# Optimization experiments

Measured on AMD Instinct MI355X. Metric: run time of the kernel, lower is better.

## Reference

```python
import jax, jax.numpy as jnp
import numpy as np

B, S, Lb, C, CP, H = 64, 4, 64, 32, 16, 4
LN_EPS = 1e-5


def layer_norm(x, g, b):
    mu = jnp.mean(x, axis=-1, keepdims=True)
    var = jnp.mean(jnp.square(x - mu), axis=-1, keepdims=True)
    return (x - mu) * jax.lax.rsqrt(var + LN_EPS) * g + b


def mha(x, w_in, b_in, w_out, b_out, h):
    # torch nn.MultiheadAttention, batch_first, self-attention
    Bx, L, Cx = x.shape
    d = Cx // h
    qkv = x @ w_in.T + b_in                      # (Bx, L, 3C)
    q, k, v = jnp.split(qkv, 3, axis=-1)
    sp = lambda t: t.reshape(Bx, L, h, d).transpose(0, 2, 1, 3)  # (Bx,h,L,d)
    q, k, v = sp(q), sp(k), sp(v)
    scale = 1.0 / jnp.sqrt(jnp.asarray(d, x.dtype))
    attn = jax.nn.softmax(jnp.einsum('bhid,bhjd->bhij', q, k) * scale, axis=-1)
    o = jnp.einsum('bhij,bhjd->bhid', attn, v).transpose(0, 2, 1, 3).reshape(Bx, L, Cx)
    return o @ w_out.T + b_out


def setup_inputs() -> dict:
    key = jax.random.key(0)
    ks = jax.random.split(key, 20)
    g = lambda i, shape, s=0.05: (jax.random.normal(ks[i], shape, dtype=jnp.float32) * s)
    inp = {
        'chip_ctcf': jax.random.normal(ks[0], (B, Lb), dtype=jnp.float32),
        'chip_hac':  jax.random.normal(ks[1], (B, Lb), dtype=jnp.float32),
        'chip_me1':  jax.random.normal(ks[2], (B, Lb), dtype=jnp.float32),
        'chip_me3':  jax.random.normal(ks[3], (B, Lb), dtype=jnp.float32),
        'embed_w': g(4, (C, 1)), 'embed_b': g(5, (C,)),
        'pos_embed': g(6, (1, 1, Lb, C), 0.02),
        'row_in_w': g(7, (3 * C, C)), 'row_in_b': g(8, (3 * C,)),
        'row_out_w': g(9, (C, C)), 'row_out_b': g(10, (C,)),
        'row_ln_g': jnp.ones((C,), jnp.float32), 'row_ln_b': jnp.zeros((C,), jnp.float32),
        'col_in_w': g(11, (3 * C, C)), 'col_in_b': g(12, (3 * C,)),
        'col_out_w': g(13, (C, C)), 'col_out_b': g(14, (C,)),
        'col_ln_g': jnp.ones((C,), jnp.float32), 'col_ln_b': jnp.zeros((C,), jnp.float32),
        'proj_w': g(15, (CP, C * C)), 'proj_b': g(16, (CP,)),
        'pln_g': jnp.ones((CP,), jnp.float32), 'pln_b': jnp.zeros((CP,), jnp.float32),
    }
    return inp


def reference(chip_ctcf, chip_hac, chip_me1, chip_me3,
              embed_w, embed_b, pos_embed,
              row_in_w, row_in_b, row_out_w, row_out_b, row_ln_g, row_ln_b,
              col_in_w, col_in_b, col_out_w, col_out_b, col_ln_g, col_ln_b,
              proj_w, proj_b, pln_g, pln_b):
    Bv = chip_ctcf.shape[0]
    signals = jnp.stack([chip_ctcf, chip_hac, chip_me1, chip_me3], axis=1)  # (B,4,64)
    # Linear(1, C): scalar embed
    msa = signals[..., None] * embed_w[:, 0] + embed_b                      # (B,4,64,C)
    msa = msa + pos_embed
    # row attention over the 64 bins, per track
    x = msa.reshape(Bv * S, Lb, C)
    x = layer_norm(x + mha(x, row_in_w, row_in_b, row_out_w, row_out_b, H), row_ln_g, row_ln_b)
    msa = x.reshape(Bv, S, Lb, C)
    # column attention over the 4 tracks, per bin
    x = msa.transpose(0, 2, 1, 3).reshape(Bv * Lb, S, C)
    x = layer_norm(x + mha(x, col_in_w, col_in_b, col_out_w, col_out_b, H), col_ln_g, col_ln_b)
    msa = x.reshape(Bv, Lb, S, C).transpose(0, 2, 1, 3)                     # (B,4,64,C)
    # outer product of the track-mean (as written in the torch source)
    m = jnp.mean(msa, axis=1)                                               # (B,64,C)
    pair = jnp.einsum('bic,bjd->bijcd', m, m).reshape(Bv, Lb, Lb, C * C)    # (B,64,64,1024)
    nrm = jnp.sqrt(jnp.sum(jnp.square(pair), axis=-1, keepdims=True))
    pair = pair / jnp.maximum(nrm, 1e-6)                                    # F.normalize eps=1e-6
    feat = pair @ proj_w.T + proj_b                                         # (B,64,64,CP)
    feat = layer_norm(feat, pln_g, pln_b)
    feat = feat * jax.nn.sigmoid(feat)                                      # SiLU
    return feat.transpose(0, 3, 1, 2)                                       # (B,CP,64,64)
```

## Files before the change

### kernel.cpp

```cpp
#include <hip/hip_runtime.h>
#include <hip/hip_bf16.h>

#define LN_EPS 1e-5f

__device__ __forceinline__ float dot8(float4 a0, float4 a1, float4 b0, float4 b1) {
    return a0.x * b0.x + a0.y * b0.y + a0.z * b0.z + a0.w * b0.w +
           a1.x * b1.x + a1.y * b1.y + a1.z * b1.z + a1.w * b1.w;
}

__global__ __launch_bounds__(256) void k_row(
    const float* __restrict__ ctcf, const float* __restrict__ hac,
    const float* __restrict__ me1,  const float* __restrict__ me3,
    const float* __restrict__ ew,   const float* __restrict__ eb,
    const float* __restrict__ pe,
    const float* __restrict__ w_in, const float* __restrict__ b_in,
    const float* __restrict__ w_out,const float* __restrict__ b_out,
    const float* __restrict__ ln_g, const float* __restrict__ ln_b,
    float* __restrict__ msaR)
{
    __shared__ float sx[64][33];
    __shared__ float sqkv[64 * 100];
    __shared__ float so[64][33];
    __shared__ float swin[96 * 32];
    __shared__ float swout[32 * 32];
    __shared__ float sbin[96];
    __shared__ float sbout[32], sg[32], sb[32];
    __shared__ float smean[64], srstd[64];

    const int blk = blockIdx.x;
    const int s   = blk & 3;
    const int b   = blk >> 2;
    const int tid = threadIdx.x;

    const float* chip = (s == 0) ? ctcf : (s == 1) ? hac : (s == 2) ? me1 : me3;

    for (int n = tid; n < 96 * 32; n += 256) swin[n] = w_in[n];
    for (int n = tid; n < 32 * 32; n += 256) swout[n] = w_out[n];
    if (tid < 96) sbin[tid] = b_in[tid];
    if (tid < 32) {
        sbout[tid] = b_out[tid];
        sg[tid] = ln_g[tid];
        sb[tid] = ln_b[tid];
    }
    for (int n = tid; n < 2048; n += 256) {
        int l = n >> 5, c = n & 31;
        sx[l][c] = chip[b * 64 + l] * ew[c] + eb[c] + pe[l * 32 + c];
    }
    __syncthreads();

    const int l  = tid & 63;
    const int cg = tid >> 6;

    float xr[32];
#pragma unroll
    for (int c = 0; c < 32; ++c) xr[c] = sx[l][c];

#pragma unroll
    for (int i = 0; i < 24; ++i) {
        int cc = i * 4 + cg;
        const float4* wr4 = (const float4*)&swin[cc * 32];
        float acc = sbin[cc];
#pragma unroll
        for (int c4 = 0; c4 < 8; ++c4) {
            float4 wv = wr4[c4];
            acc += xr[c4 * 4 + 0] * wv.x + xr[c4 * 4 + 1] * wv.y +
                   xr[c4 * 4 + 2] * wv.z + xr[c4 * 4 + 3] * wv.w;
        }
        sqkv[l * 100 + cc] = acc;
    }
    __syncthreads();

    {
        const int h = cg;
        const float4* qp = (const float4*)&sqkv[l * 100 + h * 8];
        float4 q0 = qp[0], q1 = qp[1];
        const float scale = 0.35355339059327373f;
        float mrun = -1e30f, denom = 0.f, a[8];
#pragma unroll
        for (int dd = 0; dd < 8; ++dd) a[dd] = 0.f;
        for (int j = 0; j < 64; ++j) {
            const float4* kp = (const float4*)&sqkv[j * 100 + 32 + h * 8];
            float4 k0 = kp[0], k1 = kp[1];
            float sc = dot8(q0, q1, k0, k1) * scale;
            const float4* vp = (const float4*)&sqkv[j * 100 + 64 + h * 8];
            float4 v0 = vp[0], v1 = vp[1];
            float mnew = fmaxf(mrun, sc);
            float corr = __expf(mrun - mnew);
            float w = __expf(sc - mnew);
            denom = denom * corr + w;
            a[0] = a[0] * corr + w * v0.x;  a[1] = a[1] * corr + w * v0.y;
            a[2] = a[2] * corr + w * v0.z;  a[3] = a[3] * corr + w * v0.w;
            a[4] = a[4] * corr + w * v1.x;  a[5] = a[5] * corr + w * v1.y;
            a[6] = a[6] * corr + w * v1.z;  a[7] = a[7] * corr + w * v1.w;
            mrun = mnew;
        }
        float inv = 1.f / denom;
#pragma unroll
        for (int dd = 0; dd < 8; ++dd) so[l][h * 8 + dd] = a[dd] * inv;
    }
    __syncthreads();

    {
        float orow[32];
#pragma unroll
        for (int k = 0; k < 32; ++k) orow[k] = so[l][k];
#pragma unroll
        for (int i = 0; i < 8; ++i) {
            int c = i * 4 + cg;
            const float4* wr4 = (const float4*)&swout[c * 32];
            float acc = sbout[c] + xr[c];
#pragma unroll
            for (int k4 = 0; k4 < 8; ++k4) {
                float4 wv = wr4[k4];
                acc += orow[k4 * 4 + 0] * wv.x + orow[k4 * 4 + 1] * wv.y +
                       orow[k4 * 4 + 2] * wv.z + orow[k4 * 4 + 3] * wv.w;
            }
            sqkv[l * 100 + c] = acc;
        }
    }
    __syncthreads();

    if (tid < 64) {
        float mu = 0.f;
#pragma unroll
        for (int c = 0; c < 32; ++c) mu += sqkv[tid * 100 + c];
        mu *= (1.f / 32.f);
        float var = 0.f;
#pragma unroll
        for (int c = 0; c < 32; ++c) { float d = sqkv[tid * 100 + c] - mu; var += d * d; }
        var *= (1.f / 32.f);
        smean[tid] = mu;
        srstd[tid] = rsqrtf(var + LN_EPS);
    }
    __syncthreads();

    float* outp = msaR + blk * 2048;
    for (int n = tid; n < 2048; n += 256) {
        int ll = n >> 5, c = n & 31;
        outp[n] = (sqkv[ll * 100 + c] - smean[ll]) * srstd[ll] * sg[c] + sb[c];
    }
}

__global__ __launch_bounds__(256) void k_col(
    const float* __restrict__ msaR,
    const float* __restrict__ w_in, const float* __restrict__ b_in,
    const float* __restrict__ w_out,const float* __restrict__ b_out,
    const float* __restrict__ ln_g, const float* __restrict__ ln_b,
    float* __restrict__ m_out, float* __restrict__ nrm_out)
{
    __shared__ float sx[64][33];
    __shared__ float sqkv[64 * 100];
    __shared__ float so[64][33];
    __shared__ float swi[96 * 32];
    __shared__ float swo[32 * 32];
    __shared__ float sbi[96];
    __shared__ float sbo[32], sg[32], sb[32];
    __shared__ float smean2[64], srstd2[64];
    __shared__ float smv[16][33];

    const int bx = blockIdx.x;
    const int b  = bx >> 2;
    const int l0 = (bx & 3) * 16;
    const int tid = threadIdx.x;

    for (int n = tid; n < 96 * 32; n += 256) swi[n] = w_in[n];
    for (int n = tid; n < 32 * 32; n += 256) swo[n] = w_out[n];
    if (tid < 96) sbi[tid] = b_in[tid];
    if (tid < 32) {
        sbo[tid] = b_out[tid];
        sg[tid] = ln_g[tid];
        sb[tid] = ln_b[tid];
    }
    for (int n = tid; n < 2048; n += 256) {
        int s = n >> 9, lo = (n >> 5) & 15, c = n & 31;
        sx[s * 16 + lo][c] = msaR[((b * 4 + s) * 64 + l0 + lo) * 32 + c];
    }
    __syncthreads();

    const int r  = tid & 63;
    const int sS = r & 3, lo = r >> 2;
    const int cg = tid >> 6;

    float xr[32];
#pragma unroll
    for (int c = 0; c < 32; ++c) xr[c] = sx[sS * 16 + lo][c];

#pragma unroll
    for (int i = 0; i < 24; ++i) {
        int cc = i * 4 + cg;
        const float4* wr4 = (const float4*)&swi[cc * 32];
        float acc = sbi[cc];
#pragma unroll
        for (int c4 = 0; c4 < 8; ++c4) {
            float4 wv = wr4[c4];
            acc += xr[c4 * 4 + 0] * wv.x + xr[c4 * 4 + 1] * wv.y +
                   xr[c4 * 4 + 2] * wv.z + xr[c4 * 4 + 3] * wv.w;
        }
        sqkv[r * 100 + cc] = acc;
    }
    __syncthreads();

    {
        const int la = tid >> 4, h = (tid >> 2) & 3, ia = tid & 3;
        const float scale = 0.35355339059327373f;
        const float4* qp = (const float4*)&sqkv[(la * 4 + ia) * 100 + h * 8];
        float4 q0 = qp[0], q1 = qp[1];
        float sc[4];
        float mx = -1e30f;
#pragma unroll
        for (int jj = 0; jj < 4; ++jj) {
            const float4* kp = (const float4*)&sqkv[(la * 4 + jj) * 100 + 32 + h * 8];
            sc[jj] = dot8(q0, q1, kp[0], kp[1]) * scale;
            mx = fmaxf(mx, sc[jj]);
        }
        float den = 0.f;
#pragma unroll
        for (int jj = 0; jj < 4; ++jj) { sc[jj] = __expf(sc[jj] - mx); den += sc[jj]; }
        float inv = 1.f / den;
        float a[8];
#pragma unroll
        for (int dd = 0; dd < 8; ++dd) a[dd] = 0.f;
#pragma unroll
        for (int jj = 0; jj < 4; ++jj) {
            const float4* vp = (const float4*)&sqkv[(la * 4 + jj) * 100 + 64 + h * 8];
            float4 v0 = vp[0], v1 = vp[1];
            float wgt = sc[jj];
            a[0] += wgt * v0.x;  a[1] += wgt * v0.y;
            a[2] += wgt * v0.z;  a[3] += wgt * v0.w;
            a[4] += wgt * v1.x;  a[5] += wgt * v1.y;
            a[6] += wgt * v1.z;  a[7] += wgt * v1.w;
        }
#pragma unroll
        for (int dd = 0; dd < 8; ++dd) so[la * 4 + ia][h * 8 + dd] = a[dd] * inv;
    }
    __syncthreads();

    {
        float orow[32];
#pragma unroll
        for (int k = 0; k < 32; ++k) orow[k] = so[r][k];
#pragma unroll
        for (int i = 0; i < 8; ++i) {
            int c = i * 4 + cg;
            const float4* wr4 = (const float4*)&swo[c * 32];
            float acc = sbo[c] + xr[c];
#pragma unroll
            for (int k4 = 0; k4 < 8; ++k4) {
                float4 wv = wr4[k4];
                acc += orow[k4 * 4 + 0] * wv.x + orow[k4 * 4 + 1] * wv.y +
                       orow[k4 * 4 + 2] * wv.z + orow[k4 * 4 + 3] * wv.w;
            }
            sqkv[r * 100 + c] = acc;
        }
    }
    __syncthreads();

    if (tid < 64) {
        float mu = 0.f;
#pragma unroll
        for (int c = 0; c < 32; ++c) mu += sqkv[tid * 100 + c];
        mu *= (1.f / 32.f);
        float var = 0.f;
#pragma unroll
        for (int c = 0; c < 32; ++c) { float d = sqkv[tid * 100 + c] - mu; var += d * d; }
        var *= (1.f / 32.f);
        smean2[tid] = mu;
        srstd2[tid] = rsqrtf(var + LN_EPS);
    }
    __syncthreads();

    for (int pass = 0; pass < 2; ++pass) {
        int idx = pass * 256 + tid;
        int loo = idx >> 5, c = idx & 31;
        float acc = 0.f;
#pragma unroll
        for (int ss = 0; ss < 4; ++ss) {
            int rr = loo * 4 + ss;
            acc += (sqkv[rr * 100 + c] - smean2[rr]) * srstd2[rr];
        }
        float mval = 0.25f * acc * sg[c] + sb[c];
        m_out[(b * 64 + l0 + loo) * 32 + c] = mval;
        smv[loo][c] = mval * mval;
    }
    __syncthreads();

    if (tid < 16) {
        float sum = 0.f;
#pragma unroll
        for (int c = 0; c < 32; ++c) sum += smv[tid][c];
        nrm_out[b * 64 + l0 + tid] = sqrtf(sum);
    }
}

__global__ __launch_bounds__(256) void k_pair(
    const float* __restrict__ m, const float* __restrict__ nrm,
    const float* __restrict__ pw, const float* __restrict__ pb,
    const float* __restrict__ pg, const float* __restrict__ pbeta,
    float* __restrict__ out)
{
    __shared__ float smj[64][36];
    __shared__ float sT[16 * 520];
    __shared__ float snj[64];
    __shared__ float sbias[16], sgam[16], sbet[16];

    const int bx = blockIdx.x;
    const int b  = bx >> 2;
    const int i0 = (bx & 3) * 16;
    const int tid = threadIdx.x;
    const int lane = tid & 63, w = tid >> 6;

    const float* mb = m + b * 2048;
    for (int n = tid; n < 2048; n += 256) smj[n >> 5][n & 31] = mb[n];
    if (tid < 64) snj[tid] = nrm[b * 64 + tid];
    if (tid < 16) {
        sbias[tid] = pb[tid];
        sgam[tid]  = pg[tid];
        sbet[tid]  = pbeta[tid];
    }
    __syncthreads();

    float treg[4][8];
#pragma unroll
    for (int q = 0; q < 4; ++q)
#pragma unroll
        for (int k = 0; k < 8; ++k) treg[q][k] = 0.f;
    {
        const float* pwl = pw + (lane >> 5) * 1024 + (lane & 31);
#pragma unroll 4
        for (int c = 0; c < 32; ++c) {
            float m0 = smj[i0 + w * 4 + 0][c];
            float m1 = smj[i0 + w * 4 + 1][c];
            float m2 = smj[i0 + w * 4 + 2][c];
            float m3 = smj[i0 + w * 4 + 3][c];
#pragma unroll
            for (int k = 0; k < 8; ++k) {
                float wv = pwl[k * 2048 + c * 32];
                treg[0][k] += m0 * wv;
                treg[1][k] += m1 * wv;
                treg[2][k] += m2 * wv;
                treg[3][k] += m3 * wv;
            }
        }
    }
#pragma unroll
    for (int q = 0; q < 4; ++q)
#pragma unroll
        for (int k = 0; k < 8; ++k)
            sT[(w * 4 + q) * 520 + lane + 64 * k] = treg[q][k];

    const int j = lane;
    float mj[32];
    {
        const float4* mjp = (const float4*)&smj[j][0];
#pragma unroll
        for (int d4 = 0; d4 < 8; ++d4) {
            float4 t = mjp[d4];
            mj[d4 * 4 + 0] = t.x;  mj[d4 * 4 + 1] = t.y;
            mj[d4 * 4 + 2] = t.z;  mj[d4 * 4 + 3] = t.w;
        }
    }
    const float nj = snj[j];

    for (int q = 0; q < 4; ++q) {
        const int il = w * 4 + q;
        const int ig = i0 + il;
        const float invn = 1.f / fmaxf(snj[ig] * nj, 1e-6f);
        float f[16];
#pragma unroll
        for (int cp = 0; cp < 16; ++cp) {
            const float4* tr = (const float4*)&sT[il * 520 + cp * 32];
            float acc = 0.f;
#pragma unroll
            for (int d4 = 0; d4 < 8; ++d4) {
                float4 tv = tr[d4];
                acc += tv.x * mj[d4 * 4 + 0] + tv.y * mj[d4 * 4 + 1] +
                       tv.z * mj[d4 * 4 + 2] + tv.w * mj[d4 * 4 + 3];
            }
            f[cp] = acc * invn + sbias[cp];
        }
        float mu = 0.f;
#pragma unroll
        for (int cp = 0; cp < 16; ++cp) mu += f[cp];
        mu *= (1.f / 16.f);
        float var = 0.f;
#pragma unroll
        for (int cp = 0; cp < 16; ++cp) { float d = f[cp] - mu; var += d * d; }
        var *= (1.f / 16.f);
        const float rstd = rsqrtf(var + LN_EPS);
#pragma unroll
        for (int cp = 0; cp < 16; ++cp) {
            float v = (f[cp] - mu) * rstd * sgam[cp] + sbet[cp];
            float sl = v / (1.f + __expf(-v));
            out[((b * 16 + cp) * 64 + ig) * 64 + j] = sl;
        }
    }
}

extern "C" void kernel_launch(void* const* d_in, const int* in_sizes, int n_in,
                              void* d_out, int out_size, void* d_ws, size_t ws_size,
                              hipStream_t stream) {
    const float* ctcf  = (const float*)d_in[0];
    const float* hac   = (const float*)d_in[1];
    const float* me1   = (const float*)d_in[2];
    const float* me3   = (const float*)d_in[3];
    const float* ew    = (const float*)d_in[4];
    const float* ebias = (const float*)d_in[5];
    const float* pe    = (const float*)d_in[6];
    const float* riw   = (const float*)d_in[7];
    const float* rib   = (const float*)d_in[8];
    const float* row_  = (const float*)d_in[9];
    const float* rob   = (const float*)d_in[10];
    const float* rlg   = (const float*)d_in[11];
    const float* rlb   = (const float*)d_in[12];
    const float* ciw   = (const float*)d_in[13];
    const float* cib   = (const float*)d_in[14];
    const float* cow   = (const float*)d_in[15];
    const float* cob   = (const float*)d_in[16];
    const float* clg   = (const float*)d_in[17];
    const float* clb   = (const float*)d_in[18];
    const float* pw    = (const float*)d_in[19];
    const float* pb    = (const float*)d_in[20];
    const float* pg    = (const float*)d_in[21];
    const float* pbt   = (const float*)d_in[22];

    float* out = (float*)d_out;

    float* msaR = (float*)d_out;
    float* mbuf = (float*)d_ws;
    float* nbuf = mbuf + 64 * 64 * 32;

    k_row<<<256, 256, 0, stream>>>(ctcf, hac, me1, me3, ew, ebias, pe,
                                   riw, rib, row_, rob, rlg, rlb, msaR);
    k_col<<<256, 256, 0, stream>>>(msaR, ciw, cib, cow, cob, clg, clb,
                                   mbuf, nbuf);
    k_pair<<<256, 256, 0, stream>>>(mbuf, nbuf, pw, pb, pg, pbt, out);
}
```

Before: 164.7 us.

## Split pair kernel into 8-row blocks and cache projection weights in registers

k_pair now handles 8 rows per block instead of 16, which doubles the grid to 512 blocks and halves the shared T buffer. Each thread preloads 64 projection-weight values into registers, and the T precompute is restructured so every thread computes two (cp,c) outputs for all 8 rows. A __syncthreads is added before T is consumed, and the main loop processes 2 rows per wave. The aim is more parallelism and occupancy on the pair stage, at the cost of reading the weights once per block (twice as many blocks) and higher register pressure.

```diff
diff --git a/kernel.cpp b/kernel.cpp
--- a/kernel.cpp
+++ b/kernel.cpp
@@ -299,15 +299,23 @@
     float* __restrict__ out)
 {
     __shared__ float smj[64][36];
-    __shared__ float sT[16 * 520];
+    __shared__ float sT[8 * 520];
     __shared__ float snj[64];
     __shared__ float sbias[16], sgam[16], sbet[16];
 
     const int bx = blockIdx.x;
-    const int b  = bx >> 2;
-    const int i0 = (bx & 3) * 16;
+    const int b  = bx >> 3;
+    const int i0 = (bx & 7) * 8;
     const int tid = threadIdx.x;
     const int lane = tid & 63, w = tid >> 6;
+
+    const int rem0 = lane + 128 * w;
+    const int rem1 = rem0 + 64;
+    const float* pw0 = pw + (rem0 >> 5) * 1024 + (rem0 & 31);
+    const float* pw1 = pw + (rem1 >> 5) * 1024 + (rem1 & 31);
+    float w0[32], w1[32];
+#pragma unroll
+    for (int c = 0; c < 32; ++c) { w0[c] = pw0[c * 32]; w1[c] = pw1[c * 32]; }
 
     const float* mb = m + b * 2048;
     for (int n = tid; n < 2048; n += 256) smj[n >> 5][n & 31] = mb[n];
@@ -319,34 +327,22 @@
     }
     __syncthreads();
 
-    float treg[4][8];
-#pragma unroll
-    for (int q = 0; q < 4; ++q)
-#pragma unroll
-        for (int k = 0; k < 8; ++k) treg[q][k] = 0.f;
-    {
-        const float* pwl = pw + (lane >> 5) * 1024 + (lane & 31);
-#pragma unroll 4
-        for (int c = 0; c < 32; ++c) {
-            float m0 = smj[i0 + w * 4 + 0][c];
-            float m1 = smj[i0 + w * 4 + 1][c];
-            float m2 = smj[i0 + w * 4 + 2][c];
-            float m3 = smj[i0 + w * 4 + 3][c];
-#pragma unroll
-            for (int k = 0; k < 8; ++k) {
-                float wv = pwl[k * 2048 + c * 32];
-                treg[0][k] += m0 * wv;
-                treg[1][k] += m1 * wv;
-                treg[2][k] += m2 * wv;
-                treg[3][k] += m3 * wv;
-            }
-        }
-    }
-#pragma unroll
-    for (int q = 0; q < 4; ++q)
-#pragma unroll
-        for (int k = 0; k < 8; ++k)
-            sT[(w * 4 + q) * 520 + lane + 64 * k] = treg[q][k];
+#pragma unroll
+    for (int il = 0; il < 8; ++il) {
+        const float4* mr4 = (const float4*)&smj[i0 + il][0];
+        float a0 = 0.f, a1 = 0.f;
+#pragma unroll
+        for (int c4 = 0; c4 < 8; ++c4) {
+            float4 mv = mr4[c4];
+            a0 += mv.x * w0[c4 * 4 + 0] + mv.y * w0[c4 * 4 + 1] +
+                  mv.z * w0[c4 * 4 + 2] + mv.w * w0[c4 * 4 + 3];
+            a1 += mv.x * w1[c4 * 4 + 0] + mv.y * w1[c4 * 4 + 1] +
+                  mv.z * w1[c4 * 4 + 2] + mv.w * w1[c4 * 4 + 3];
+        }
+        sT[il * 520 + rem0] = a0;
+        sT[il * 520 + rem1] = a1;
+    }
+    __syncthreads();
 
     const int j = lane;
     float mj[32];
@@ -361,8 +357,9 @@
     }
     const float nj = snj[j];
 
-    for (int q = 0; q < 4; ++q) {
-        const int il = w * 4 + q;
+#pragma unroll
+    for (int q = 0; q < 2; ++q) {
+        const int il = w * 2 + q;
         const int ig = i0 + il;
         const float invn = 1.f / fmaxf(snj[ig] * nj, 1e-6f);
         float f[16];
@@ -433,5 +430,5 @@
                                    riw, rib, row_, rob, rlg, rlb, msaR);
     k_col<<<256, 256, 0, stream>>>(msaR, ciw, cib, cow, cob, clg, clb,
                                    mbuf, nbuf);
-    k_pair<<<256, 256, 0, stream>>>(mbuf, nbuf, pw, pb, pg, pbt, out);
+    k_pair<<<512, 256, 0, stream>>>(mbuf, nbuf, pw, pb, pg, pbt, out);
 }
```

After: 157.0 us. 4.7% less time.
